# Kernel optimization log

Measured on AMD Instinct MI355X. Metric: run time of the kernel, lower is better.

The kernel has to match this reference:

```python
import jax, jax.numpy as jnp
import numpy as np

SIGMA = 0.05
SIGMA2 = SIGMA * SIGMA
N_NODES = 100000
N_EDGES = 3200000


def setup_inputs() -> dict:
    key = jax.random.key(0)
    k1, k2, k3, k4 = jax.random.split(key, 4)
    source_points = jax.random.normal(k1, (N_NODES, 3), dtype=jnp.float32)
    target_points = jax.random.normal(k2, (N_NODES, 3), dtype=jnp.float32)
    edge_index = jax.random.randint(k3, (2, N_EDGES), 0, N_NODES, dtype=jnp.int64)
    edge_weights = jax.random.uniform(k4, (N_EDGES, 1), dtype=jnp.float32)
    return {"source_points": source_points, "target_points": target_points,
            "edge_index": edge_index, "edge_weights": edge_weights}


def reference(source_points, target_points, edge_index, edge_weights):
    N = source_points.shape[0]
    dst = edge_index[0]  # center point each edge contributes to
    nbr = edge_index[1]  # neighbor point index

    src_nb = source_points[nbr]            # [E,3]
    tgt_nb = target_points[nbr]            # [E,3]

    ones_e = jnp.ones((edge_index.shape[1],), dtype=source_points.dtype)
    counts = jnp.maximum(jax.ops.segment_sum(ones_e, dst, num_segments=N), 1.0)[:, None]
    src_centers = jax.ops.segment_sum(src_nb, dst, num_segments=N) / counts  # [N,3]
    tgt_centers = jax.ops.segment_sum(tgt_nb, dst, num_segments=N) / counts  # [N,3]

    src_diff = (src_nb - src_centers[dst]) * edge_weights  # [E,3]
    tgt_diff = tgt_nb - tgt_centers[dst]                   # [E,3]

    # per-edge outer product, scattered to per-point 3x3 covariances
    edge_mats = src_diff[:, :, None] * tgt_diff[:, None, :]          # [E,3,3]
    point_mats = jax.ops.segment_sum(edge_mats, dst, num_segments=N)  # [N,3,3]

    U, S, Vh = jnp.linalg.svd(point_mats)  # torch.svd's V = Vh^T, so U @ V^T == U @ Vh
    R0 = jnp.matmul(U, Vh)
    det = jnp.linalg.det(R0)
    ones_n = jnp.ones((N,), dtype=source_points.dtype)
    d_diag = jax.lax.stop_gradient(jnp.stack([ones_n, ones_n, det], axis=-1))  # [N,3]
    R = jnp.matmul(U * d_diag[:, None, :], Vh)  # U @ diag(d) @ Vh, proper rotation

    trans = tgt_centers - jnp.einsum('nij,nj->ni', R, src_centers)  # [N,3]

    # apply each neighbor's rigid transform and compute robust weights
    transformed = jnp.einsum('eij,ej->ei', R[nbr], src_nb) + trans[nbr]  # [E,3]
    d2 = jnp.sum(jnp.square(transformed - tgt_nb), axis=-1, keepdims=True)  # [E,1]
    new_edge_weights = SIGMA2 / (d2 + SIGMA2)
    return (R, trans, new_edge_weights)
```

## Files before the change

### kernel.cpp

```cpp
#include <hip/hip_runtime.h>
#include <math.h>

static constexpr float kSigma2 = 0.05f * 0.05f;
static constexpr int kCap = 6400;

__device__ __forceinline__ int load_idx(const void* ei, long long j, int is64) {
    if (is64) return (int)(((const long long*)ei)[j]);
    return ((const int*)ei)[j];
}

__global__ void k_detect(const int* __restrict__ ei32, int E, int* __restrict__ nz) {
    int t = threadIdx.x;
    int lim = E < 2048 ? E : 2048;
    int acc = 0;
    for (int k = t; k < lim; k += blockDim.x) acc |= ei32[2 * k + 1];
    if (acc) atomicOr(nz, 1);
}

__global__ void k_pack(const float* __restrict__ src, const float* __restrict__ tgt,
                       float4* __restrict__ s4, float4* __restrict__ t4, int N) {
    int i = blockIdx.x * blockDim.x + threadIdx.x;
    if (i >= N) return;
    s4[i] = make_float4(src[3 * i + 0], src[3 * i + 1], src[3 * i + 2], 0.0f);
    t4[i] = make_float4(tgt[3 * i + 0], tgt[3 * i + 1], tgt[3 * i + 2], 0.0f);
}

__device__ void kabsch_from_M(const double M[3][3], double Rm[3][3]) {
    Rm[0][0] = 1; Rm[0][1] = 0; Rm[0][2] = 0;
    Rm[1][0] = 0; Rm[1][1] = 1; Rm[1][2] = 0;
    Rm[2][0] = 0; Rm[2][1] = 0; Rm[2][2] = 1;

    double frob2 = 0.0;
#pragma unroll
    for (int r = 0; r < 3; ++r)
#pragma unroll
        for (int c = 0; c < 3; ++c) frob2 += M[r][c] * M[r][c];
    if (frob2 <= 1e-80) return;

    double A[3][3];
#pragma unroll
    for (int r = 0; r < 3; ++r)
#pragma unroll
        for (int c = 0; c < 3; ++c) {
            double s = 0.0;
#pragma unroll
            for (int k = 0; k < 3; ++k) s += M[k][r] * M[k][c];
            A[r][c] = s;
        }
    double V[3][3] = {{1, 0, 0}, {0, 1, 0}, {0, 0, 1}};
    const int PL[3] = {0, 0, 1};
    const int QL[3] = {1, 2, 2};
    for (int sweep = 0; sweep < 15; ++sweep) {
        double off = fabs(A[0][1]) + fabs(A[0][2]) + fabs(A[1][2]);
        if (off == 0.0) break;
        for (int pi = 0; pi < 3; ++pi) {
            int p = PL[pi], q = QL[pi], r3 = 3 - p - q;
            double apq = A[p][q];
            if (apq == 0.0) continue;
            double theta = (A[q][q] - A[p][p]) / (2.0 * apq);
            double t = copysign(1.0, theta) / (fabs(theta) + sqrt(theta * theta + 1.0));
            double c = 1.0 / sqrt(t * t + 1.0);
            double s = t * c;
            A[p][p] -= t * apq;
            A[q][q] += t * apq;
            A[p][q] = 0.0; A[q][p] = 0.0;
            double arp = A[r3][p], arq = A[r3][q];
            A[r3][p] = c * arp - s * arq; A[p][r3] = A[r3][p];
            A[r3][q] = s * arp + c * arq; A[q][r3] = A[r3][q];
#pragma unroll
            for (int k = 0; k < 3; ++k) {
                double vp = V[k][p], vq = V[k][q];
                V[k][p] = c * vp - s * vq;
                V[k][q] = s * vp + c * vq;
            }
        }
    }
    double lam[3] = {A[0][0], A[1][1], A[2][2]};
    int id0 = 0, id1 = 1, id2 = 2, tt;
    if (lam[id0] < lam[id1]) { tt = id0; id0 = id1; id1 = tt; }
    if (lam[id0] < lam[id2]) { tt = id0; id0 = id2; id2 = tt; }
    if (lam[id1] < lam[id2]) { tt = id1; id1 = id2; id2 = tt; }
    double v1[3] = {V[0][id0], V[1][id0], V[2][id0]};
    double v2[3] = {V[0][id1], V[1][id1], V[2][id1]};
    double v3[3] = {V[0][id2], V[1][id2], V[2][id2]};

    double b1[3], b2[3];
#pragma unroll
    for (int r = 0; r < 3; ++r) {
        b1[r] = M[r][0] * v1[0] + M[r][1] * v1[1] + M[r][2] * v1[2];
        b2[r] = M[r][0] * v2[0] + M[r][1] * v2[1] + M[r][2] * v2[2];
    }
    double n1 = sqrt(b1[0] * b1[0] + b1[1] * b1[1] + b1[2] * b1[2]);
    if (n1 <= 1e-150) return;
    double u1[3] = {b1[0] / n1, b1[1] / n1, b1[2] / n1};
    double dot = u1[0] * b2[0] + u1[1] * b2[1] + u1[2] * b2[2];
    double w2[3] = {b2[0] - dot * u1[0], b2[1] - dot * u1[1], b2[2] - dot * u1[2]};
    double n2 = sqrt(w2[0] * w2[0] + w2[1] * w2[1] + w2[2] * w2[2]);
    double u2[3];
    if (n2 > n1 * 1e-12) {
        u2[0] = w2[0] / n2; u2[1] = w2[1] / n2; u2[2] = w2[2] / n2;
    } else {
        double ex0 = (fabs(u1[0]) < 0.9) ? 1.0 : 0.0;
        double ex1 = 1.0 - ex0;
        double cx = u1[1] * 0.0 - u1[2] * ex1;
        double cy = u1[2] * ex0 - u1[0] * 0.0;
        double cz = u1[0] * ex1 - u1[1] * ex0;
        double cn = sqrt(cx * cx + cy * cy + cz * cz);
        u2[0] = cx / cn; u2[1] = cy / cn; u2[2] = cz / cn;
    }
    double u3[3] = {u1[1] * u2[2] - u1[2] * u2[1],
                    u1[2] * u2[0] - u1[0] * u2[2],
                    u1[0] * u2[1] - u1[1] * u2[0]};
    double dV = v1[0] * (v2[1] * v3[2] - v2[2] * v3[1])
              - v1[1] * (v2[0] * v3[2] - v2[2] * v3[0])
              + v1[2] * (v2[0] * v3[1] - v2[1] * v3[0]);
    dV = (dV >= 0.0) ? 1.0 : -1.0;
#pragma unroll
    for (int r = 0; r < 3; ++r)
#pragma unroll
        for (int c = 0; c < 3; ++c)
            Rm[r][c] = u1[r] * v1[c] + u2[r] * v2[c] + dV * u3[r] * v3[c];
}


__global__ void __launch_bounds__(256) k_bhist(const void* __restrict__ ei,
                                               int* __restrict__ btot16,
                                               const int* __restrict__ nz,
                                               int E, int N, int nbuckets) {
    __shared__ int lhist[1024];
    int t = threadIdx.x;
    long long tile = (long long)blockIdx.x * 16384;
    long long remll = (long long)E - tile;
    int rem = (remll < 16384) ? (int)remll : 16384;
    int is64 = (*nz == 0);
    for (int i = t; i < 1024; i += 256) lhist[i] = 0;
    __syncthreads();
    if (rem == 16384) {
        for (int it = 0; it < 8; ++it) {
            long long base = tile + (long long)it * 2048 + (long long)t * 8;
            int d[8];
            if (is64) {
                const long long* p = (const long long*)ei + base;
#pragma unroll
                for (int k = 0; k < 4; ++k) {
                    longlong2 v = ((const longlong2*)p)[k];
                    d[2 * k] = (int)v.x;
                    d[2 * k + 1] = (int)v.y;
                }
            } else {
                const int* p = (const int*)ei + base;
                int4 a = ((const int4*)p)[0];
                int4 bb = ((const int4*)p)[1];
                d[0] = a.x; d[1] = a.y; d[2] = a.z; d[3] = a.w;
                d[4] = bb.x; d[5] = bb.y; d[6] = bb.z; d[7] = bb.w;
            }
#pragma unroll
            for (int k = 0; k < 8; ++k)
                if ((unsigned)d[k] < (unsigned)N) atomicAdd(&lhist[d[k] >> 7], 1);
        }
    } else {
        for (int idx = t; idx < rem; idx += 256) {
            int d = load_idx(ei, tile + idx, is64);
            if ((unsigned)d < (unsigned)N) atomicAdd(&lhist[d >> 7], 1);
        }
    }
    __syncthreads();
    for (int b = t; b < 1024; b += 256) {
        int c = lhist[b];
        if (c > 0 && b < nbuckets) atomicAdd(&btot16[b * 16], c);
    }
}

__global__ void k_scan(const int* __restrict__ btot16, int* __restrict__ boff,
                       int* __restrict__ cur16, int* __restrict__ curC16, int nbuckets) {
    __shared__ int sm[1024];
    int t = threadIdx.x;
    int v = (t < nbuckets) ? btot16[t * 16] : 0;
    sm[t] = v;
    __syncthreads();
    for (int s = 1; s < 1024; s <<= 1) {
        int x = (t >= s) ? sm[t - s] : 0;
        __syncthreads();
        sm[t] += x;
        __syncthreads();
    }
    if (t < nbuckets) {
        int excl = sm[t] - v;
        boff[t] = excl;
        cur16[t * 16] = excl;
        if ((t & 63) == 0) curC16[(t >> 6) * 16] = excl;
    }
    if (t == nbuckets - 1) boff[nbuckets] = sm[t];
}

__global__ void __launch_bounds__(256) k_cscatter(const void* __restrict__ ei,
                                                  const float* __restrict__ ew,
                                                  int* __restrict__ curC16,
                                                  int2* __restrict__ sedge1,
                                                  const int* __restrict__ nz,
                                                  int E, int N, int ncoarse) {
    __shared__ int2 stage[2048];
    __shared__ unsigned char binOf[2048];
    __shared__ int hist[16];
    __shared__ int excl[16];
    __shared__ int gbase[16];
    int t = threadIdx.x;
    long long tile = (long long)blockIdx.x * 2048;
    long long remll = (long long)E - tile;
    int rem = (remll < 2048) ? (int)remll : 2048;
    int is64 = (*nz == 0);
    if (t < 16) hist[t] = 0;
    __syncthreads();

    int dd[8], nn[8];
    float ww[8];
    int cnt8 = 0;
    if (rem == 2048) {
        if (is64) {
            const long long* pd = (const long long*)ei + tile + (long long)t * 8;
            const long long* pn = (const long long*)ei + (long long)E + tile + (long long)t * 8;
#pragma unroll
            for (int k = 0; k < 4; ++k) {
                longlong2 vd = ((const longlong2*)pd)[k];
                longlong2 vn = ((const longlong2*)pn)[k];
                dd[2 * k] = (int)vd.x; dd[2 * k + 1] = (int)vd.y;
                nn[2 * k] = (int)vn.x; nn[2 * k + 1] = (int)vn.y;
            }
        } else {
            const int* pd = (const int*)ei + tile + (long long)t * 8;
            const int* pn = (const int*)ei + (long long)E + tile + (long long)t * 8;
            int4 a = ((const int4*)pd)[0], b = ((const int4*)pd)[1];
            int4 c = ((const int4*)pn)[0], d = ((const int4*)pn)[1];
            dd[0] = a.x; dd[1] = a.y; dd[2] = a.z; dd[3] = a.w;
            dd[4] = b.x; dd[5] = b.y; dd[6] = b.z; dd[7] = b.w;
            nn[0] = c.x; nn[1] = c.y; nn[2] = c.z; nn[3] = c.w;
            nn[4] = d.x; nn[5] = d.y; nn[6] = d.z; nn[7] = d.w;
        }
        const float* pw = ew + tile + (long long)t * 8;
        float4 wa = ((const float4*)pw)[0], wb = ((const float4*)pw)[1];
        ww[0] = wa.x; ww[1] = wa.y; ww[2] = wa.z; ww[3] = wa.w;
        ww[4] = wb.x; ww[5] = wb.y; ww[6] = wb.z; ww[7] = wb.w;
        cnt8 = 8;
    } else {
        int base = t * 8;
#pragma unroll
        for (int k = 0; k < 8; ++k) {
            int idx = base + k;
            if (idx < rem) {
                long long e = tile + idx;
                dd[cnt8] = load_idx(ei, e, is64);
                nn[cnt8] = load_idx(ei, (long long)E + e, is64);
                ww[cnt8] = ew[e];
                ++cnt8;
            }
        }
    }

    int mybin[8], myrank[8];
    int2 mypay[8];
#pragma unroll
    for (int k = 0; k < 8; ++k) {
        mybin[k] = -1;
        if (k < cnt8) {
            int d = dd[k];
            if ((unsigned)d < (unsigned)N) {
                int n = nn[k];
                if ((unsigned)n >= (unsigned)N) n = N;
                int cb = d >> 13;
                mybin[k] = cb;
                myrank[k] = atomicAdd(&hist[cb], 1);
                mypay[k].x = (n << 13) | (d & 8191);
                mypay[k].y = __float_as_int(ww[k]);
            }
        }
    }
    __syncthreads();
    if (t == 0) {
        int run = 0;
#pragma unroll
        for (int c = 0; c < 16; ++c) { excl[c] = run; run += hist[c]; }
    }
    __syncthreads();
#pragma unroll
    for (int k = 0; k < 8; ++k) {
        if (mybin[k] >= 0) {
            int lpos = excl[mybin[k]] + myrank[k];
            stage[lpos] = mypay[k];
            binOf[lpos] = (unsigned char)mybin[k];
        }
    }
    if (t < 16) {
        int c = hist[t];
        gbase[t] = (c > 0 && t < ncoarse) ? atomicAdd(&curC16[t * 16], c) : 0;
    }
    __syncthreads();
    int total = excl[15] + hist[15];
    for (int lpos = t; lpos < total; lpos += 256) {
        int c = binOf[lpos];
        sedge1[gbase[c] + (lpos - excl[c])] = stage[lpos];
    }
}

__global__ void __launch_bounds__(256) k_fscatter(const int2* __restrict__ sedge1,
                                                  int* __restrict__ cur16,
                                                  const int* __restrict__ boff,
                                                  int2* __restrict__ sedge2,
                                                  int E, int nbuckets, int ncoarse) {
    __shared__ int2 stage[2048];
    __shared__ unsigned short binOf[2048];
    __shared__ int lhist[1024];
    __shared__ int lincl[1024];
    __shared__ int gbase[1024];
    __shared__ int co[17];
    int t = threadIdx.x;
    if (t <= ncoarse) {
        int f = t * 64;
        if (f > nbuckets) f = nbuckets;
        co[t] = boff[f];
    }
    for (int i = t; i < 1024; i += 256) lhist[i] = 0;
    __syncthreads();
    int Ev = co[ncoarse];
    long long tile = (long long)blockIdx.x * 2048;
    if (tile >= Ev) return;
    long long remll = (long long)Ev - tile;
    int rem = (remll < 2048) ? (int)remll : 2048;

    int2 pay[8];
    int cnt8 = 0;
    if (rem == 2048) {
        const int4* p4 = (const int4*)(sedge1 + tile + (long long)t * 8);
#pragma unroll
        for (int k = 0; k < 4; ++k) {
            int4 v = p4[k];
            pay[2 * k].x = v.x; pay[2 * k].y = v.y;
            pay[2 * k + 1].x = v.z; pay[2 * k + 1].y = v.w;
        }
        cnt8 = 8;
    } else {
        int base = t * 8;
#pragma unroll
        for (int k = 0; k < 8; ++k) {
            int idx = base + k;
            if (idx < rem) pay[cnt8++] = sedge1[tile + idx];
        }
    }

    int mybin[8], myrank[8];
    int2 mypay[8];
#pragma unroll
    for (int k = 0; k < 8; ++k) {
        mybin[k] = -1;
        if (k < cnt8) {
            long long pos = tile + t * 8 + k;
            int c = 0;
            while (c + 1 < ncoarse && pos >= co[c + 1]) ++c;
            int x1 = pay[k].x;
            unsigned nbr = ((unsigned)x1) >> 13;
            int fin = c * 64 + ((x1 & 8191) >> 7);
            mybin[k] = fin;
            myrank[k] = atomicAdd(&lhist[fin], 1);
            mypay[k].x = (int)((nbr << 7) | (unsigned)(x1 & 127));
            mypay[k].y = pay[k].y;
        }
    }
    __syncthreads();
    for (int i = t; i < 1024; i += 256) lincl[i] = lhist[i];
    __syncthreads();
    for (int s = 1; s < 1024; s <<= 1) {
        int tmp[4];
#pragma unroll
        for (int j = 0; j < 4; ++j) {
            int i = (j << 8) + t;
            tmp[j] = (i >= s) ? lincl[i - s] : 0;
        }
        __syncthreads();
#pragma unroll
        for (int j = 0; j < 4; ++j) {
            int i = (j << 8) + t;
            lincl[i] += tmp[j];
        }
        __syncthreads();
    }
#pragma unroll
    for (int k = 0; k < 8; ++k) {
        if (mybin[k] >= 0) {
            int ex = lincl[mybin[k]] - lhist[mybin[k]];
            int lpos = ex + myrank[k];
            stage[lpos] = mypay[k];
            binOf[lpos] = (unsigned short)mybin[k];
        }
    }
    __syncthreads();
    for (int bb = t; bb < 1024; bb += 256) {
        int c = lhist[bb];
        gbase[bb] = (c > 0 && bb < nbuckets) ? atomicAdd(&cur16[bb * 16], c) : 0;
    }
    __syncthreads();
    int total = lincl[1023];
    for (int lpos = t; lpos < total; lpos += 256) {
        int bb = binOf[lpos];
        int ex = lincl[bb] - lhist[bb];
        sedge2[gbase[bb] + (lpos - ex)] = stage[lpos];
    }
}

__global__ void __launch_bounds__(256) k_binscatter(const void* __restrict__ ei,
                                                    const float* __restrict__ ew,
                                                    int* __restrict__ cur16,
                                                    int2* __restrict__ sedge,
                                                    const int* __restrict__ nz,
                                                    int E, int N, int nbuckets) {
    __shared__ int2 stage[2048];
    __shared__ unsigned short binOf[2048];
    __shared__ int lhist[1024];
    __shared__ int lincl[1024];
    __shared__ int gbase[1024];
    int t = threadIdx.x;
    long long tile = (long long)blockIdx.x * 2048;
    long long remll = (long long)E - tile;
    int rem = (remll < 2048) ? (int)remll : 2048;
    int is64 = (*nz == 0);
    for (int i = t; i < 1024; i += 256) lhist[i] = 0;
    __syncthreads();

    int dd[8], nn[8];
    float ww[8];
    int cnt8 = 0;
    if (rem == 2048) {
        if (is64) {
            const long long* pd = (const long long*)ei + tile + (long long)t * 8;
            const long long* pn = (const long long*)ei + (long long)E + tile + (long long)t * 8;
#pragma unroll
            for (int k = 0; k < 4; ++k) {
                longlong2 vd = ((const longlong2*)pd)[k];
                longlong2 vn = ((const longlong2*)pn)[k];
                dd[2 * k] = (int)vd.x; dd[2 * k + 1] = (int)vd.y;
                nn[2 * k] = (int)vn.x; nn[2 * k + 1] = (int)vn.y;
            }
        } else {
            const int* pd = (const int*)ei + tile + (long long)t * 8;
            const int* pn = (const int*)ei + (long long)E + tile + (long long)t * 8;
            int4 a = ((const int4*)pd)[0], b = ((const int4*)pd)[1];
            int4 c = ((const int4*)pn)[0], d = ((const int4*)pn)[1];
            dd[0] = a.x; dd[1] = a.y; dd[2] = a.z; dd[3] = a.w;
            dd[4] = b.x; dd[5] = b.y; dd[6] = b.z; dd[7] = b.w;
            nn[0] = c.x; nn[1] = c.y; nn[2] = c.z; nn[3] = c.w;
            nn[4] = d.x; nn[5] = d.y; nn[6] = d.z; nn[7] = d.w;
        }
        const float* pw = ew + tile + (long long)t * 8;
        float4 wa = ((const float4*)pw)[0], wb = ((const float4*)pw)[1];
        ww[0] = wa.x; ww[1] = wa.y; ww[2] = wa.z; ww[3] = wa.w;
        ww[4] = wb.x; ww[5] = wb.y; ww[6] = wb.z; ww[7] = wb.w;
        cnt8 = 8;
    } else {
        int base = t * 8;
#pragma unroll
        for (int k = 0; k < 8; ++k) {
            int idx = base + k;
            if (idx < rem) {
                long long e = tile + idx;
                dd[cnt8] = load_idx(ei, e, is64);
                nn[cnt8] = load_idx(ei, (long long)E + e, is64);
                ww[cnt8] = ew[e];
                ++cnt8;
            }
        }
    }

    int mybin[8];
    int myrank[8];
    int2 mypay[8];
#pragma unroll
    for (int k = 0; k < 8; ++k) {
        mybin[k] = -1;
        if (k < cnt8) {
            int d = dd[k];
            if ((unsigned)d < (unsigned)N) {
                int n = nn[k];
                if ((unsigned)n >= (unsigned)N) n = N;
                int bb = d >> 7;
                mybin[k] = bb;
                myrank[k] = atomicAdd(&lhist[bb], 1);
                mypay[k].x = (n << 7) | (d & 127);
                mypay[k].y = __float_as_int(ww[k]);
            }
        }
    }
    __syncthreads();
    for (int i = t; i < 1024; i += 256) lincl[i] = lhist[i];
    __syncthreads();
    for (int s = 1; s < 1024; s <<= 1) {
        int tmp[4];
#pragma unroll
        for (int j = 0; j < 4; ++j) {
            int i = (j << 8) + t;
            tmp[j] = (i >= s) ? lincl[i - s] : 0;
        }
        __syncthreads();
#pragma unroll
        for (int j = 0; j < 4; ++j) {
            int i = (j << 8) + t;
            lincl[i] += tmp[j];
        }
        __syncthreads();
    }
#pragma unroll
    for (int k = 0; k < 8; ++k) {
        if (mybin[k] >= 0) {
            int ex = lincl[mybin[k]] - lhist[mybin[k]];
            int lpos = ex + myrank[k];
            stage[lpos] = mypay[k];
            binOf[lpos] = (unsigned short)mybin[k];
        }
    }
    __syncthreads();
    for (int bb = t; bb < 1024; bb += 256) {
        int c = lhist[bb];
        gbase[bb] = (c > 0 && bb < nbuckets) ? atomicAdd(&cur16[bb * 16], c) : 0;
    }
    __syncthreads();
    int total = lincl[1023];
    for (int lpos = t; lpos < total; lpos += 256) {
        int bb = binOf[lpos];
        int ex = lincl[bb] - lhist[bb];
        sedge[gbase[bb] + (lpos - ex)] = stage[lpos];
    }
}

__global__ void __launch_bounds__(256) k_sort(const int* __restrict__ boff,
                                              int2* __restrict__ sedge,
                                              int2* __restrict__ nseg) {
    __shared__ int2 sorted[kCap];
    __shared__ int hist[128];
    __shared__ int scanbuf[128];
    __shared__ int offs[128];
    __shared__ int cur[128];
    int b = blockIdx.x, t = threadIdx.x;
    int e0 = boff[b], e1 = boff[b + 1];
    int cnt = e1 - e0;
    if (t < 128) hist[t] = 0;
    __syncthreads();
    if (cnt <= kCap) {
        for (int i = t; i < cnt; i += 256)
            atomicAdd(&hist[sedge[e0 + i].x & 127], 1);
        __syncthreads();
        if (t < 128) scanbuf[t] = hist[t];
        __syncthreads();
        for (int s = 1; s < 128; s <<= 1) {
            int v = 0;
            if (t < 128 && t >= s) v = scanbuf[t - s];
            __syncthreads();
            if (t < 128) scanbuf[t] += v;
            __syncthreads();
        }
        if (t < 128) {
            int ex = scanbuf[t] - hist[t];
            offs[t] = ex;
            cur[t] = ex;
        }
        __syncthreads();
        for (int i = t; i < cnt; i += 256) {
            int2 p = sedge[e0 + i];
            int r = atomicAdd(&cur[p.x & 127], 1);
            sorted[r] = p;
        }
        __syncthreads();
        for (int i = t; i < cnt; i += 256) sedge[e0 + i] = sorted[i];
        if (t < 128) nseg[b * 128 + t] = make_int2(e0 + offs[t], hist[t]);
    } else {
        if (t < 128) nseg[b * 128 + t] = make_int2(e0, -cnt);
    }
}

__global__ void __launch_bounds__(256) k_moment(const int2* __restrict__ nseg,
                                                const int2* __restrict__ sedge,
                                                const float4* __restrict__ s4,
                                                const float4* __restrict__ t4,
                                                float* __restrict__ Rout,
                                                float* __restrict__ Tout,
                                                float* __restrict__ wnode, int N) {
    __shared__ float acc[23][128];
    int b = blockIdx.x, t = threadIdx.x;
    int oct = t >> 3, lane8 = t & 7;
    for (int node = oct; node < 128; node += 32) {
        int2 seg = nseg[b * 128 + node];
        float v[23];
#pragma unroll
        for (int i = 0; i < 23; ++i) v[i] = 0.0f;
        int start = seg.x;
        int cn = seg.y;
        int total = (cn >= 0) ? cn : -cn;
        int filter = (cn < 0);
        for (int j = lane8; j < total; j += 8) {
            int2 p = sedge[start + j];
            if (filter && (p.x & 127) != node) continue;
            unsigned n = ((unsigned)p.x) >> 7;
            if (n >= (unsigned)N) continue;
            float w = __int_as_float(p.y);
            float4 a = s4[n];
            float4 bb = t4[n];
            float sx = a.x, sy = a.y, sz = a.z;
            float tx = bb.x, ty = bb.y, tz = bb.z;
            v[0] += 1.0f;
            v[1] += sx; v[2] += sy; v[3] += sz;
            v[4] += tx; v[5] += ty; v[6] += tz;
            v[7] += w;
            float wsx = w * sx, wsy = w * sy, wsz = w * sz;
            v[8] += wsx; v[9] += wsy; v[10] += wsz;
            v[11] += w * tx; v[12] += w * ty; v[13] += w * tz;
            v[14] += wsx * tx; v[15] += wsx * ty; v[16] += wsx * tz;
            v[17] += wsy * tx; v[18] += wsy * ty; v[19] += wsy * tz;
            v[20] += wsz * tx; v[21] += wsz * ty; v[22] += wsz * tz;
        }
#pragma unroll
        for (int m = 1; m < 8; m <<= 1) {
#pragma unroll
            for (int i = 0; i < 23; ++i) v[i] += __shfl_xor(v[i], m, 64);
        }
        if (lane8 == 0) {
#pragma unroll
            for (int i = 0; i < 23; ++i) acc[i][node] = v[i];
        }
    }
    __syncthreads();
    if (t < 128) {
        long long i = (long long)b * 128 + t;
        if (i < N) {
            double cntv = (double)acc[0][t];
            double inv = 1.0 / fmax(cntv, 1.0);
            double sb0 = acc[1][t] * inv, sb1 = acc[2][t] * inv, sb2 = acc[3][t] * inv;
            double tb0 = acc[4][t] * inv, tb1 = acc[5][t] * inv, tb2 = acc[6][t] * inv;
            double Sw = acc[7][t];
            double Sws[3] = {acc[8][t], acc[9][t], acc[10][t]};
            double Swt[3] = {acc[11][t], acc[12][t], acc[13][t]};
            double sb[3] = {sb0, sb1, sb2}, tb[3] = {tb0, tb1, tb2};
            double M[3][3];
#pragma unroll
            for (int r = 0; r < 3; ++r)
#pragma unroll
                for (int c = 0; c < 3; ++c)
                    M[r][c] = (double)acc[14 + 3 * r + c][t]
                            - sb[r] * Swt[c] - Sws[r] * tb[c] + Sw * sb[r] * tb[c];
            double Rm[3][3];
            kabsch_from_M(M, Rm);
            double T0 = tb0 - (Rm[0][0] * sb0 + Rm[0][1] * sb1 + Rm[0][2] * sb2);
            double T1 = tb1 - (Rm[1][0] * sb0 + Rm[1][1] * sb1 + Rm[1][2] * sb2);
            double T2 = tb2 - (Rm[2][0] * sb0 + Rm[2][1] * sb1 + Rm[2][2] * sb2);
#pragma unroll
            for (int r = 0; r < 3; ++r)
#pragma unroll
                for (int c = 0; c < 3; ++c)
                    Rout[9 * i + 3 * r + c] = (float)Rm[r][c];
            Tout[3 * i + 0] = (float)T0;
            Tout[3 * i + 1] = (float)T1;
            Tout[3 * i + 2] = (float)T2;
            float4 a = s4[(int)i];
            float4 q = t4[(int)i];
            double x0 = Rm[0][0] * a.x + Rm[0][1] * a.y + Rm[0][2] * a.z + T0;
            double x1 = Rm[1][0] * a.x + Rm[1][1] * a.y + Rm[1][2] * a.z + T1;
            double x2 = Rm[2][0] * a.x + Rm[2][1] * a.y + Rm[2][2] * a.z + T2;
            double d0 = x0 - q.x, d1 = x1 - q.y, d2 = x2 - q.z;
            double dd = d0 * d0 + d1 * d1 + d2 * d2;
            wnode[i] = (float)((double)kSigma2 / (dd + (double)kSigma2));
        }
    }
}

__global__ void __launch_bounds__(256) k_wgather(const void* __restrict__ ei,
                                                 const float* __restrict__ wnode,
                                                 float* __restrict__ wout,
                                                 const int* __restrict__ nz,
                                                 int E, int N) {
    int gid = blockIdx.x * blockDim.x + threadIdx.x;
    long long base = (long long)gid * 8;
    if (base >= E) return;
    int is64 = (*nz == 0);
    int n_[8];
    int full = (base + 8 <= (long long)E);
    if (full) {
        if (is64) {
            const long long* p = (const long long*)ei + (long long)E + base;
#pragma unroll
            for (int k = 0; k < 4; ++k) {
                longlong2 a = ((const longlong2*)p)[k];
                n_[2 * k] = (int)a.x;
                n_[2 * k + 1] = (int)a.y;
            }
        } else {
            const int* p = (const int*)ei + (long long)E + base;
            int4 a = ((const int4*)p)[0];
            int4 b = ((const int4*)p)[1];
            n_[0] = a.x; n_[1] = a.y; n_[2] = a.z; n_[3] = a.w;
            n_[4] = b.x; n_[5] = b.y; n_[6] = b.z; n_[7] = b.w;
        }
        float w[8];
#pragma unroll
        for (int k = 0; k < 8; ++k)
            w[k] = ((unsigned)n_[k] < (unsigned)N) ? wnode[n_[k]] : 1.0f;
        *(float4*)(wout + base) = make_float4(w[0], w[1], w[2], w[3]);
        *(float4*)(wout + base + 4) = make_float4(w[4], w[5], w[6], w[7]);
    } else {
#pragma unroll
        for (int k = 0; k < 8; ++k) {
            long long e = base + k;
            if (e < E) {
                int n = load_idx(ei, (long long)E + e, is64);
                wout[e] = ((unsigned)n < (unsigned)N) ? wnode[n] : 1.0f;
            }
        }
    }
}


__global__ void k_accum1(const void* __restrict__ ei, const float* __restrict__ src,
                         const float* __restrict__ tgt, float* __restrict__ cnt,
                         float* __restrict__ ssum, float* __restrict__ tsum,
                         const int* __restrict__ nz, int E, int N) {
    int e = blockIdx.x * blockDim.x + threadIdx.x;
    if (e >= E) return;
    int is64 = (*nz == 0);
    int d = load_idx(ei, e, is64);
    int n = load_idx(ei, (long long)E + e, is64);
    if ((unsigned)d >= (unsigned)N || (unsigned)n >= (unsigned)N) return;
    atomicAdd(&cnt[d], 1.0f);
    atomicAdd(&ssum[3 * d + 0], src[3 * n + 0]);
    atomicAdd(&ssum[3 * d + 1], src[3 * n + 1]);
    atomicAdd(&ssum[3 * d + 2], src[3 * n + 2]);
    atomicAdd(&tsum[3 * d + 0], tgt[3 * n + 0]);
    atomicAdd(&tsum[3 * d + 1], tgt[3 * n + 1]);
    atomicAdd(&tsum[3 * d + 2], tgt[3 * n + 2]);
}

__global__ void k_centers(float* __restrict__ cnt, float* __restrict__ ssum,
                          float* __restrict__ tsum, int N) {
    int i = blockIdx.x * blockDim.x + threadIdx.x;
    if (i >= N) return;
    float inv = 1.0f / fmaxf(cnt[i], 1.0f);
    ssum[3 * i + 0] *= inv; ssum[3 * i + 1] *= inv; ssum[3 * i + 2] *= inv;
    tsum[3 * i + 0] *= inv; tsum[3 * i + 1] *= inv; tsum[3 * i + 2] *= inv;
}

__global__ void k_accum2(const void* __restrict__ ei, const float* __restrict__ src,
                         const float* __restrict__ tgt, const float* __restrict__ ew,
                         const float* __restrict__ sc, const float* __restrict__ tc,
                         float* __restrict__ Mm, const int* __restrict__ nz, int E, int N) {
    int e = blockIdx.x * blockDim.x + threadIdx.x;
    if (e >= E) return;
    int is64 = (*nz == 0);
    int d = load_idx(ei, e, is64);
    int n = load_idx(ei, (long long)E + e, is64);
    if ((unsigned)d >= (unsigned)N || (unsigned)n >= (unsigned)N) return;
    float w = ew[e];
    float a0 = (src[3 * n + 0] - sc[3 * d + 0]) * w;
    float a1 = (src[3 * n + 1] - sc[3 * d + 1]) * w;
    float a2 = (src[3 * n + 2] - sc[3 * d + 2]) * w;
    float b0 = tgt[3 * n + 0] - tc[3 * d + 0];
    float b1 = tgt[3 * n + 1] - tc[3 * d + 1];
    float b2 = tgt[3 * n + 2] - tc[3 * d + 2];
    float* Md = Mm + 9 * (long long)d;
    atomicAdd(Md + 0, a0 * b0); atomicAdd(Md + 1, a0 * b1); atomicAdd(Md + 2, a0 * b2);
    atomicAdd(Md + 3, a1 * b0); atomicAdd(Md + 4, a1 * b1); atomicAdd(Md + 5, a1 * b2);
    atomicAdd(Md + 6, a2 * b0); atomicAdd(Md + 7, a2 * b1); atomicAdd(Md + 8, a2 * b2);
}

__global__ void k_kabsch(const float* __restrict__ Mm, const float* __restrict__ sc,
                         const float* __restrict__ tc, float* __restrict__ Rout,
                         float* __restrict__ Tout, int N) {
    int i = blockIdx.x * blockDim.x + threadIdx.x;
    if (i >= N) return;
    double M[3][3];
#pragma unroll
    for (int r = 0; r < 3; ++r)
#pragma unroll
        for (int c = 0; c < 3; ++c)
            M[r][c] = (double)Mm[9 * (long long)i + 3 * r + c];
    double Rm[3][3];
    kabsch_from_M(M, Rm);
    double s0 = sc[3 * i + 0], s1 = sc[3 * i + 1], s2 = sc[3 * i + 2];
    double t0 = tc[3 * i + 0], t1 = tc[3 * i + 1], t2 = tc[3 * i + 2];
#pragma unroll
    for (int r = 0; r < 3; ++r)
#pragma unroll
        for (int c = 0; c < 3; ++c)
            Rout[9 * (long long)i + 3 * r + c] = (float)Rm[r][c];
    Tout[3 * i + 0] = (float)(t0 - (Rm[0][0] * s0 + Rm[0][1] * s1 + Rm[0][2] * s2));
    Tout[3 * i + 1] = (float)(t1 - (Rm[1][0] * s0 + Rm[1][1] * s1 + Rm[1][2] * s2));
    Tout[3 * i + 2] = (float)(t2 - (Rm[2][0] * s0 + Rm[2][1] * s1 + Rm[2][2] * s2));
}

__global__ void k_weights_plain(const void* __restrict__ ei,
                                const float* __restrict__ src,
                                const float* __restrict__ tgt,
                                const float* __restrict__ R,
                                const float* __restrict__ T,
                                float* __restrict__ wout,
                                const int* __restrict__ nz, int E, int N) {
    int e = blockIdx.x * blockDim.x + threadIdx.x;
    if (e >= E) return;
    int is64 = (*nz == 0);
    int n = load_idx(ei, (long long)E + e, is64);
    float w = 1.0f;
    if ((unsigned)n < (unsigned)N) {
        float p0 = src[3 * n + 0], p1 = src[3 * n + 1], p2 = src[3 * n + 2];
        float q0 = tgt[3 * n + 0], q1 = tgt[3 * n + 1], q2 = tgt[3 * n + 2];
        const float* Rn = R + 9 * (long long)n;
        const float* Tn = T + 3 * (long long)n;
        float x0 = Rn[0] * p0 + Rn[1] * p1 + Rn[2] * p2 + Tn[0];
        float x1 = Rn[3] * p0 + Rn[4] * p1 + Rn[5] * p2 + Tn[1];
        float x2 = Rn[6] * p0 + Rn[7] * p1 + Rn[8] * p2 + Tn[2];
        float d0 = x0 - q0, d1 = x1 - q1, d2 = x2 - q2;
        float dd = d0 * d0 + d1 * d1 + d2 * d2;
        w = kSigma2 / (dd + kSigma2);
    }
    wout[e] = w;
}

extern "C" void kernel_launch(void* const* d_in, const int* in_sizes, int n_in,
                              void* d_out, int out_size, void* d_ws, size_t ws_size,
                              hipStream_t stream) {
    const float* src = (const float*)d_in[0];
    const float* tgt = (const float*)d_in[1];
    const void* ei = d_in[2];
    const float* ew = (const float*)d_in[3];
    int N = in_sizes[0] / 3;
    int E = in_sizes[3];

    float* out = (float*)d_out;
    float* Rout = out;
    float* Tout = out + (size_t)9 * N;
    float* Wout = out + (size_t)12 * N;

    int eb = (E + 255) / 256;
    int nb = (N + 255) / 256;
    int nbuckets = (N + 127) / 128;
    int ncoarse = (nbuckets + 63) / 64;
    int tiles = (int)(((long long)E + 2047) / 2048);
    int tiles16 = (int)(((long long)E + 16383) / 16384);
    int wb8 = (int)(((long long)E + 2047) / 2048);

    size_t ctrl_ints = 16 + (size_t)nbuckets * 16 * 2 + 256 + (nbuckets + 1);
    ctrl_ints = (ctrl_ints + 3) & ~(size_t)3;
    size_t after1 = ctrl_ints + 2 * (size_t)E;
    after1 = (after1 + 3) & ~(size_t)3;
    size_t after2 = after1 + 2 * (size_t)E;
    after2 = (after2 + 3) & ~(size_t)3;
    size_t tail_ints = 8 * (size_t)N + (size_t)N + 2 * (size_t)128 * nbuckets;
    size_t needA = (after2 + tail_ints) * sizeof(int);
    size_t needB = (after1 + tail_ints) * sizeof(int);

    if (N <= 131072 && nbuckets <= 1024 && ws_size >= needB) {
        int twolevel = (ws_size >= needA) ? 1 : 0;
        int* nz = (int*)d_ws;
        int* btot16 = nz + 16;
        int* cur16 = btot16 + (size_t)nbuckets * 16;
        int* curC16 = cur16 + (size_t)nbuckets * 16;
        int* boff = curC16 + 256;
        int2* sedge1 = (int2*)((int*)d_ws + ctrl_ints);
        size_t tail_base = twolevel ? after2 : after1;
        int2* sedge2 = twolevel ? (int2*)((int*)d_ws + after1) : sedge1;
        float4* s4 = (float4*)((int*)d_ws + tail_base);
        float4* t4 = s4 + N;
        float* wnode = (float*)(t4 + N);
        int2* nseg = (int2*)(wnode + N);

        hipMemsetAsync(d_ws, 0, ctrl_ints * sizeof(int), stream);

        k_detect<<<1, 256, 0, stream>>>((const int*)ei, E, nz);
        k_pack<<<nb, 256, 0, stream>>>(src, tgt, s4, t4, N);
        k_bhist<<<tiles16, 256, 0, stream>>>(ei, btot16, nz, E, N, nbuckets);
        k_scan<<<1, 1024, 0, stream>>>(btot16, boff, cur16, curC16, nbuckets);
        if (twolevel) {
            k_cscatter<<<tiles, 256, 0, stream>>>(ei, ew, curC16, sedge1, nz, E, N, ncoarse);
            k_fscatter<<<tiles, 256, 0, stream>>>(sedge1, cur16, boff, sedge2, E, nbuckets, ncoarse);
        } else {
            k_binscatter<<<tiles, 256, 0, stream>>>(ei, ew, cur16, sedge2, nz, E, N, nbuckets);
        }
        k_sort<<<nbuckets, 256, 0, stream>>>(boff, sedge2, nseg);
        k_moment<<<nbuckets, 256, 0, stream>>>(nseg, sedge2, s4, t4, Rout, Tout, wnode, N);
        k_wgather<<<wb8, 256, 0, stream>>>(ei, wnode, Wout, nz, E, N);
    } else {
        float* cnt = (float*)d_ws;
        float* ssum = cnt + N;
        float* tsum = ssum + 3 * (size_t)N;
        float* Mm = tsum + 3 * (size_t)N;
        int* nz = (int*)(Mm + 9 * (size_t)N);
        size_t ws_bytes = (size_t)16 * N * sizeof(float) + 16;
        hipMemsetAsync(d_ws, 0, ws_bytes, stream);
        k_detect<<<1, 256, 0, stream>>>((const int*)ei, E, nz);
        k_accum1<<<eb, 256, 0, stream>>>(ei, src, tgt, cnt, ssum, tsum, nz, E, N);
        k_centers<<<nb, 256, 0, stream>>>(cnt, ssum, tsum, N);
        k_accum2<<<eb, 256, 0, stream>>>(ei, src, tgt, ew, ssum, tsum, Mm, nz, E, N);
        k_kabsch<<<nb, 256, 0, stream>>>(Mm, ssum, tsum, Rout, Tout, N);
        k_weights_plain<<<eb, 256, 0, stream>>>(ei, src, tgt, Rout, Tout, Wout, nz, E, N);
    }
}
```

Measured before the change: 279.3 us.

## Split moment accumulation from Kabsch solve and shrink fscatter histogram to tile's coarse range

k_fscatter now sizes its local histogram, prefix scan and global atomic reservation to the fine buckets inside the coarse range its tile spans, instead of always processing 1024 bins. k_moment now covers 64 nodes per block and writes its 23 per-node moments to global memory. A separate per-node kernel then does the double-precision Kabsch/SVD and weight computation with one node per thread. The aim is less wasted scan and atomic work per tile, and better occupancy because the heavy Kabsch math no longer runs in only 128 threads of each moment block. The cost is an extra launch and a 23×N float round trip through global memory.

```diff
diff --git a/kernel.cpp b/kernel.cpp
--- a/kernel.cpp
+++ b/kernel.cpp
@@ -312,13 +312,13 @@
     __shared__ int lincl[1024];
     __shared__ int gbase[1024];
     __shared__ int co[17];
+    __shared__ int s_clo, s_W;
     int t = threadIdx.x;
     if (t <= ncoarse) {
         int f = t * 64;
         if (f > nbuckets) f = nbuckets;
         co[t] = boff[f];
     }
-    for (int i = t; i < 1024; i += 256) lhist[i] = 0;
     __syncthreads();
     int Ev = co[ncoarse];
     long long tile = (long long)blockIdx.x * 2048;
@@ -326,6 +326,20 @@
     long long remll = (long long)Ev - tile;
     int rem = (remll < 2048) ? (int)remll : 2048;
 
+    if (t == 0) {
+        long long p0 = tile, p1 = tile + rem - 1;
+        int c0 = 0;
+        while (c0 + 1 < ncoarse && p0 >= co[c0 + 1]) ++c0;
+        int c1 = c0;
+        while (c1 + 1 < ncoarse && p1 >= co[c1 + 1]) ++c1;
+        s_clo = c0;
+        s_W = (c1 - c0 + 1) * 64;
+    }
+    __syncthreads();
+    int clo = s_clo, W = s_W;
+    for (int i = t; i < W; i += 256) lhist[i] = 0;
+    __syncthreads();
+
     int2 pay[8];
     int cnt8 = 0;
     if (rem == 2048) {
@@ -353,33 +367,27 @@
         mybin[k] = -1;
         if (k < cnt8) {
             long long pos = tile + t * 8 + k;
-            int c = 0;
+            int c = clo;
             while (c + 1 < ncoarse && pos >= co[c + 1]) ++c;
             int x1 = pay[k].x;
             unsigned nbr = ((unsigned)x1) >> 13;
-            int fin = c * 64 + ((x1 & 8191) >> 7);
-            mybin[k] = fin;
-            myrank[k] = atomicAdd(&lhist[fin], 1);
+            int rel = (c - clo) * 64 + ((x1 & 8191) >> 7);
+            mybin[k] = rel;
+            myrank[k] = atomicAdd(&lhist[rel], 1);
             mypay[k].x = (int)((nbr << 7) | (unsigned)(x1 & 127));
             mypay[k].y = pay[k].y;
         }
     }
     __syncthreads();
-    for (int i = t; i < 1024; i += 256) lincl[i] = lhist[i];
-    __syncthreads();
-    for (int s = 1; s < 1024; s <<= 1) {
+    for (int i = t; i < W; i += 256) lincl[i] = lhist[i];
+    __syncthreads();
+    for (int s = 1; s < W; s <<= 1) {
         int tmp[4];
-#pragma unroll
-        for (int j = 0; j < 4; ++j) {
-            int i = (j << 8) + t;
-            tmp[j] = (i >= s) ? lincl[i - s] : 0;
-        }
+        int cj = 0;
+        for (int i = t; i < W; i += 256) tmp[cj++] = (i >= s) ? lincl[i - s] : 0;
         __syncthreads();
-#pragma unroll
-        for (int j = 0; j < 4; ++j) {
-            int i = (j << 8) + t;
-            lincl[i] += tmp[j];
-        }
+        cj = 0;
+        for (int i = t; i < W; i += 256) lincl[i] += tmp[cj++];
         __syncthreads();
     }
 #pragma unroll
@@ -392,16 +400,17 @@
         }
     }
     __syncthreads();
-    for (int bb = t; bb < 1024; bb += 256) {
-        int c = lhist[bb];
-        gbase[bb] = (c > 0 && bb < nbuckets) ? atomicAdd(&cur16[bb * 16], c) : 0;
-    }
-    __syncthreads();
-    int total = lincl[1023];
+    for (int rel = t; rel < W; rel += 256) {
+        int c = lhist[rel];
+        int fin = clo * 64 + rel;
+        gbase[rel] = (c > 0 && fin < nbuckets) ? atomicAdd(&cur16[fin * 16], c) : 0;
+    }
+    __syncthreads();
+    int total = lincl[W - 1];
     for (int lpos = t; lpos < total; lpos += 256) {
-        int bb = binOf[lpos];
-        int ex = lincl[bb] - lhist[bb];
-        sedge2[gbase[bb] + (lpos - ex)] = stage[lpos];
+        int rel = binOf[lpos];
+        int ex = lincl[rel] - lhist[rel];
+        sedge2[gbase[rel] + (lpos - ex)] = stage[lpos];
     }
 }
 
@@ -577,14 +586,13 @@
                                                 const int2* __restrict__ sedge,
                                                 const float4* __restrict__ s4,
                                                 const float4* __restrict__ t4,
-                                                float* __restrict__ Rout,
-                                                float* __restrict__ Tout,
-                                                float* __restrict__ wnode, int N) {
-    __shared__ float acc[23][128];
+                                                float* __restrict__ momG, int N) {
     int b = blockIdx.x, t = threadIdx.x;
     int oct = t >> 3, lane8 = t & 7;
-    for (int node = oct; node < 128; node += 32) {
-        int2 seg = nseg[b * 128 + node];
+    int base = b * 64;
+    for (int node = base + oct; node < base + 64; node += 32) {
+        if (node >= N) break;
+        int2 seg = nseg[node];
         float v[23];
 #pragma unroll
         for (int i = 0; i < 23; ++i) v[i] = 0.0f;
@@ -592,9 +600,10 @@
         int cn = seg.y;
         int total = (cn >= 0) ? cn : -cn;
         int filter = (cn < 0);
+        int nlow = node & 127;
         for (int j = lane8; j < total; j += 8) {
             int2 p = sedge[start + j];
-            if (filter && (p.x & 127) != node) continue;
+            if (filter && (p.x & 127) != nlow) continue;
             unsigned n = ((unsigned)p.x) >> 7;
             if (n >= (unsigned)N) continue;
             float w = __int_as_float(p.y);
@@ -620,51 +629,57 @@
         }
         if (lane8 == 0) {
 #pragma unroll
-            for (int i = 0; i < 23; ++i) acc[i][node] = v[i];
-        }
-    }
-    __syncthreads();
-    if (t < 128) {
-        long long i = (long long)b * 128 + t;
-        if (i < N) {
-            double cntv = (double)acc[0][t];
-            double inv = 1.0 / fmax(cntv, 1.0);
-            double sb0 = acc[1][t] * inv, sb1 = acc[2][t] * inv, sb2 = acc[3][t] * inv;
-            double tb0 = acc[4][t] * inv, tb1 = acc[5][t] * inv, tb2 = acc[6][t] * inv;
-            double Sw = acc[7][t];
-            double Sws[3] = {acc[8][t], acc[9][t], acc[10][t]};
-            double Swt[3] = {acc[11][t], acc[12][t], acc[13][t]};
-            double sb[3] = {sb0, sb1, sb2}, tb[3] = {tb0, tb1, tb2};
-            double M[3][3];
-#pragma unroll
-            for (int r = 0; r < 3; ++r)
-#pragma unroll
-                for (int c = 0; c < 3; ++c)
-                    M[r][c] = (double)acc[14 + 3 * r + c][t]
-                            - sb[r] * Swt[c] - Sws[r] * tb[c] + Sw * sb[r] * tb[c];
-            double Rm[3][3];
-            kabsch_from_M(M, Rm);
-            double T0 = tb0 - (Rm[0][0] * sb0 + Rm[0][1] * sb1 + Rm[0][2] * sb2);
-            double T1 = tb1 - (Rm[1][0] * sb0 + Rm[1][1] * sb1 + Rm[1][2] * sb2);
-            double T2 = tb2 - (Rm[2][0] * sb0 + Rm[2][1] * sb1 + Rm[2][2] * sb2);
-#pragma unroll
-            for (int r = 0; r < 3; ++r)
-#pragma unroll
-                for (int c = 0; c < 3; ++c)
-                    Rout[9 * i + 3 * r + c] = (float)Rm[r][c];
-            Tout[3 * i + 0] = (float)T0;
-            Tout[3 * i + 1] = (float)T1;
-            Tout[3 * i + 2] = (float)T2;
-            float4 a = s4[(int)i];
-            float4 q = t4[(int)i];
-            double x0 = Rm[0][0] * a.x + Rm[0][1] * a.y + Rm[0][2] * a.z + T0;
-            double x1 = Rm[1][0] * a.x + Rm[1][1] * a.y + Rm[1][2] * a.z + T1;
-            double x2 = Rm[2][0] * a.x + Rm[2][1] * a.y + Rm[2][2] * a.z + T2;
-            double d0 = x0 - q.x, d1 = x1 - q.y, d2 = x2 - q.z;
-            double dd = d0 * d0 + d1 * d1 + d2 * d2;
-            wnode[i] = (float)((double)kSigma2 / (dd + (double)kSigma2));
-        }
-    }
+            for (int i = 0; i < 23; ++i) momG[(size_t)i * N + node] = v[i];
+        }
+    }
+}
+
+__global__ void __launch_bounds__(256) k_kabsch2(const float* __restrict__ momG,
+                                                 const float4* __restrict__ s4,
+                                                 const float4* __restrict__ t4,
+                                                 float* __restrict__ Rout,
+                                                 float* __restrict__ Tout,
+                                                 float* __restrict__ wnode, int N) {
+    int i = blockIdx.x * blockDim.x + threadIdx.x;
+    if (i >= N) return;
+    float m[23];
+#pragma unroll
+    for (int k = 0; k < 23; ++k) m[k] = momG[(size_t)k * N + i];
+    double cntv = (double)m[0];
+    double inv = 1.0 / fmax(cntv, 1.0);
+    double sb[3] = {m[1] * inv, m[2] * inv, m[3] * inv};
+    double tb[3] = {m[4] * inv, m[5] * inv, m[6] * inv};
+    double Sw = m[7];
+    double Sws[3] = {m[8], m[9], m[10]};
+    double Swt[3] = {m[11], m[12], m[13]};
+    double M[3][3];
+#pragma unroll
+    for (int r = 0; r < 3; ++r)
+#pragma unroll
+        for (int c = 0; c < 3; ++c)
+            M[r][c] = (double)m[14 + 3 * r + c]
+                    - sb[r] * Swt[c] - Sws[r] * tb[c] + Sw * sb[r] * tb[c];
+    double Rm[3][3];
+    kabsch_from_M(M, Rm);
+    double T0 = tb[0] - (Rm[0][0] * sb[0] + Rm[0][1] * sb[1] + Rm[0][2] * sb[2]);
+    double T1 = tb[1] - (Rm[1][0] * sb[0] + Rm[1][1] * sb[1] + Rm[1][2] * sb[2]);
+    double T2 = tb[2] - (Rm[2][0] * sb[0] + Rm[2][1] * sb[1] + Rm[2][2] * sb[2]);
+#pragma unroll
+    for (int r = 0; r < 3; ++r)
+#pragma unroll
+        for (int c = 0; c < 3; ++c)
+            Rout[9 * (long long)i + 3 * r + c] = (float)Rm[r][c];
+    Tout[3 * i + 0] = (float)T0;
+    Tout[3 * i + 1] = (float)T1;
+    Tout[3 * i + 2] = (float)T2;
+    float4 a = s4[i];
+    float4 q = t4[i];
+    double x0 = Rm[0][0] * a.x + Rm[0][1] * a.y + Rm[0][2] * a.z + T0;
+    double x1 = Rm[1][0] * a.x + Rm[1][1] * a.y + Rm[1][2] * a.z + T1;
+    double x2 = Rm[2][0] * a.x + Rm[2][1] * a.y + Rm[2][2] * a.z + T2;
+    double d0 = x0 - q.x, d1 = x1 - q.y, d2 = x2 - q.z;
+    double dd = d0 * d0 + d1 * d1 + d2 * d2;
+    wnode[i] = (float)((double)kSigma2 / (dd + (double)kSigma2));
 }
 
 __global__ void __launch_bounds__(256) k_wgather(const void* __restrict__ ei,
@@ -833,6 +848,7 @@
 
     int eb = (E + 255) / 256;
     int nb = (N + 255) / 256;
+    int nb64 = (N + 63) / 64;
     int nbuckets = (N + 127) / 128;
     int ncoarse = (nbuckets + 63) / 64;
     int tiles = (int)(((long long)E + 2047) / 2048);
@@ -845,7 +861,8 @@
     after1 = (after1 + 3) & ~(size_t)3;
     size_t after2 = after1 + 2 * (size_t)E;
     after2 = (after2 + 3) & ~(size_t)3;
-    size_t tail_ints = 8 * (size_t)N + (size_t)N + 2 * (size_t)128 * nbuckets;
+    size_t tail_ints = 8 * (size_t)N + (size_t)N + 23 * (size_t)N
+                     + 2 * (size_t)128 * nbuckets;
     size_t needA = (after2 + tail_ints) * sizeof(int);
     size_t needB = (after1 + tail_ints) * sizeof(int);
 
@@ -862,7 +879,8 @@
         float4* s4 = (float4*)((int*)d_ws + tail_base);
         float4* t4 = s4 + N;
         float* wnode = (float*)(t4 + N);
-        int2* nseg = (int2*)(wnode + N);
+        float* momG = wnode + N;
+        int2* nseg = (int2*)(momG + 23 * (size_t)N);
 
         hipMemsetAsync(d_ws, 0, ctrl_ints * sizeof(int), stream);
 
@@ -877,7 +895,8 @@
             k_binscatter<<<tiles, 256, 0, stream>>>(ei, ew, cur16, sedge2, nz, E, N, nbuckets);
         }
         k_sort<<<nbuckets, 256, 0, stream>>>(boff, sedge2, nseg);
-        k_moment<<<nbuckets, 256, 0, stream>>>(nseg, sedge2, s4, t4, Rout, Tout, wnode, N);
+        k_moment<<<nb64, 256, 0, stream>>>(nseg, sedge2, s4, t4, momG, N);
+        k_kabsch2<<<nb, 256, 0, stream>>>(momG, s4, t4, Rout, Tout, wnode, N);
         k_wgather<<<wb8, 256, 0, stream>>>(ei, wnode, Wout, nz, E, N);
     } else {
         float* cnt = (float*)d_ws;
```

New measurement: 272.1 us. 1.03x faster.
